# Optimization experiments

Hardware: AMD Instinct MI355X
Metric: run time of the kernel (lower is better)

The kernel has to match this reference:

```python
import jax, jax.numpy as jnp
import numpy as np

B, C, L, D = 8, 16, 512, 256  # batch, channels (attended axis), seq len, d_model


def setup_inputs() -> dict:
    key = jax.random.key(0)
    ks = jax.random.split(key, 9)
    d = D
    x = jax.random.normal(ks[0], (B, C, L, D), dtype=jnp.float32)
    # qkv projection: Linear(d, 3d), xavier_normal weight, zero-ish bias
    Wqkv = jax.random.normal(ks[1], (3 * d, d), dtype=jnp.float32) * (2.0 / (4 * d)) ** 0.5
    bqkv = jnp.zeros((3 * d,), dtype=jnp.float32)
    # additive-attention scorer V: Linear(d, 1)
    Vw = jax.random.normal(ks[2], (1, d), dtype=jnp.float32) * (1.0 / d) ** 0.5
    Vb = jnp.zeros((1,), dtype=jnp.float32)
    bh = jnp.zeros((d,), dtype=jnp.float32)  # nn.Parameter(torch.zeros(d_model))
    ba = jnp.zeros((1,), dtype=jnp.float32)  # nn.Parameter(torch.zeros(1))
    # output projection Linear(d, d)
    Wout = jax.random.normal(ks[3], (d, d), dtype=jnp.float32) * (1.0 / d) ** 0.5
    bout = jnp.zeros((d,), dtype=jnp.float32)
    return {"x": x, "Wqkv": Wqkv, "bqkv": bqkv, "Vw": Vw, "Vb": Vb,
            "bh": bh, "ba": ba, "Wout": Wout, "bout": bout}


def reference(x, Wqkv, bqkv, Vw, Vb, bh, ba, Wout, bout):
    b, c, l, d = x.shape
    # (b, c, l, d) -> (b*l, c, d): attention over the channel axis c per position
    xf = jnp.transpose(x, (0, 2, 1, 3)).reshape(b * l, c, d)
    qkv = xf @ Wqkv.T + bqkv                       # (B, c, 3d)
    q, k, v = jnp.split(qkv, 3, axis=-1)           # each (B, c, d)
    # additive (Bahdanau) score: V(tanh(q_i + k_j + bh)) + ba
    h = jnp.tanh(q[:, :, None, :] + k[:, None, :, :] + bh)  # (B, c, c, d)
    score = jnp.einsum('bqkd,d->bqk', h, Vw[0]) + Vb[0] + ba[0]  # (B, c, c)
    A = jax.nn.softmax(score, axis=-1)             # stable softmax (matches exp(s-max)/sum)
    # torch einsum 'b c c, b c d -> b c d': repeated index -> DIAGONAL of A scales v
    z = jnp.einsum('bcc,bcd->bcd', A, v)           # (B, c, d)
    z = z.reshape(b, l, c, d).transpose(0, 2, 1, 3)  # (b, c, l, d)
    return z @ Wout.T + bout
```

## Files before the change

kernel.cpp:

```cpp
#include <hip/hip_runtime.h>


typedef __attribute__((ext_vector_type(8))) short bf16x8;
typedef __attribute__((ext_vector_type(4))) float f32x4;
typedef __attribute__((ext_vector_type(8))) _Float16 h16x8;
typedef __attribute__((ext_vector_type(4))) _Float16 h16x4;
typedef const __attribute__((address_space(1))) void* gp1_t;
typedef __attribute__((address_space(3))) void* lp3_t;

__device__ __forceinline__ unsigned short f2bf(float f) {
  union { float f; unsigned int u; } v; v.f = f;
  return (unsigned short)((v.u + 0x7FFFu + ((v.u >> 16) & 1u)) >> 16);
}

__device__ __forceinline__ unsigned int cvt_pk_bf16(float a, float b) {
  unsigned int r;
  asm("v_cvt_pk_bf16_f32 %0, %1, %2" : "=v"(r) : "v"(a), "v"(b));
  return r;
}

__global__ __launch_bounds__(256) void ca_prep_kernel(
    const float* __restrict__ Wqkv, const float* __restrict__ Wout,
    const float* __restrict__ bqkv, const float* __restrict__ bh,
    unsigned short* __restrict__ Wqb_t, unsigned short* __restrict__ Wcb_t,
    float* __restrict__ bcomb, float* __restrict__ bsc) {
  const int blk = blockIdx.x;
  if (blk < 64) {
    const int t = blk * 256 + threadIdx.x;
    const int k8 = t >> 9, n = t & 511;
    const float* src = Wqkv + (size_t)n * 256 + k8 * 8;
    const float4 v0 = *(const float4*)src;
    const float4 v1 = *(const float4*)(src + 4);
    bf16x8 o;
    o[0] = (short)f2bf(v0.x); o[1] = (short)f2bf(v0.y);
    o[2] = (short)f2bf(v0.z); o[3] = (short)f2bf(v0.w);
    o[4] = (short)f2bf(v1.x); o[5] = (short)f2bf(v1.y);
    o[6] = (short)f2bf(v1.z); o[7] = (short)f2bf(v1.w);
    *(bf16x8*)(Wqb_t + (size_t)t * 8) = o;
    return;
  }
  const int dp = blk - 64;
  const int e = threadIdx.x;
  if (dp < 2) {
    const int n = dp * 256 + e;
    const float b = bqkv[n] + (n < 256 ? bh[n] : 0.f);
    bsc[n] = b * 2.8853900817779268f;
  }
  const float* wrow = Wout + (size_t)dp * 256;
  float acc = 0.f;
  for (int f = 0; f < 256; ++f)
    acc = fmaf(wrow[f], Wqkv[(size_t)(512 + f) * 256 + e], acc);
  Wcb_t[((size_t)(e >> 3) * 256 + dp) * 8 + (e & 7)] = f2bf(acc);
  if (e == 0) {
    float b = 0.f;
    for (int f = 0; f < 256; ++f) b = fmaf(wrow[f], bqkv[512 + f], b);
    bcomb[dp] = b;
  }
}

__global__ __launch_bounds__(512, 6) void ca_fused(
    const float* __restrict__ x,
    const unsigned short* __restrict__ Wqb_t,
    const unsigned short* __restrict__ Wcb_t,
    const float* __restrict__ bsc,
    const float* __restrict__ Vw,
    const float* __restrict__ bcomb, const float* __restrict__ bout,
    float* __restrict__ out) {
  __shared__ __align__(16) unsigned short xs[32 * 264];
  __shared__ __align__(16) unsigned short BsEs[16640];
  __shared__ __align__(16) float vw_s[256];
  __shared__ float af_s[32];
  unsigned short* const Bs = BsEs;
  _Float16* const Es = (_Float16*)BsEs;

  const int tid = threadIdx.x;
  const int lane = tid & 63, wave = tid >> 6;
  const int quad = lane >> 4, l15 = lane & 15;
  const int rt0 = blockIdx.x * 32;

  if (tid < 256) vw_s[tid] = -2.f * Vw[tid];

#pragma unroll
  for (int i = 0; i < 4; ++i) {
    const int sb = wave * 256 + i * 64;
    const unsigned short* g = Wqb_t + (size_t)(sb + lane) * 8;
    __builtin_amdgcn_global_load_lds((gp1_t)g, (lp3_t)(Bs + sb * 8), 16, 0, 0);
  }

  {
    const int rl = tid >> 4, c0 = (tid & 15) * 16;
    const int r = rt0 + rl;
    const int b = r >> 13, l = (r >> 4) & 511, c = r & 15;
    const float* src = x + ((size_t)(b * 16 + c) * 512 + l) * 256 + c0;
    unsigned short* dst = xs + rl * 264 + c0;
#pragma unroll
    for (int j = 0; j < 2; ++j) {
      const float4 v0 = *(const float4*)(src + j * 8);
      const float4 v1 = *(const float4*)(src + j * 8 + 4);
      uint4 o;
      o.x = cvt_pk_bf16(v0.x, v0.y);
      o.y = cvt_pk_bf16(v0.z, v0.w);
      o.z = cvt_pk_bf16(v1.x, v1.y);
      o.w = cvt_pk_bf16(v1.z, v1.w);
      *(uint4*)(dst + j * 8) = o;
    }
  }
  __syncthreads();

  f32x4 acc[2][4] = {};
  for (int k0c = 0; k0c < 8; ++k0c) {
    bf16x8 af[2], bfr[4];
#pragma unroll
    for (int mi = 0; mi < 2; ++mi)
      af[mi] = *(const bf16x8*)&xs[(mi * 16 + l15) * 264 + k0c * 32 + quad * 8];
#pragma unroll
    for (int ni = 0; ni < 4; ++ni)
      bfr[ni] = *(const bf16x8*)&Bs[(quad * 512 + wave * 64 + ni * 16 + l15) * 8];
    __syncthreads();
    if (k0c < 7) {
#pragma unroll
      for (int i = 0; i < 4; ++i) {
        const int sb = wave * 256 + i * 64;
        const unsigned short* g =
            Wqb_t + ((size_t)(k0c + 1) * 2048 + sb + lane) * 8;
        __builtin_amdgcn_global_load_lds((gp1_t)g, (lp3_t)(Bs + sb * 8), 16, 0, 0);
      }
    }
#pragma unroll
    for (int mi = 0; mi < 2; ++mi)
#pragma unroll
      for (int ni = 0; ni < 4; ++ni)
        acc[mi][ni] = __builtin_amdgcn_mfma_f32_16x16x32_bf16(
            bfr[ni], af[mi], acc[mi][ni], 0, 0, 0);
    __syncthreads();
  }

  const float SC = 2.8853900817779268f;
#pragma unroll
  for (int mi = 0; mi < 2; ++mi) {
    const int rl = mi * 16 + l15;
#pragma unroll
    for (int ni = 0; ni < 4; ++ni) {
      const int n = wave * 64 + ni * 16 + quad * 4;
      const float4 bs = *(const float4*)(bsc + n);
      h16x4 st;
      st[0] = (_Float16)__builtin_amdgcn_exp2f(
          fminf(15.f, fmaxf(-15.f, fmaf(acc[mi][ni][0], SC, bs.x))));
      st[1] = (_Float16)__builtin_amdgcn_exp2f(
          fminf(15.f, fmaxf(-15.f, fmaf(acc[mi][ni][1], SC, bs.y))));
      st[2] = (_Float16)__builtin_amdgcn_exp2f(
          fminf(15.f, fmaxf(-15.f, fmaf(acc[mi][ni][2], SC, bs.z))));
      st[3] = (_Float16)__builtin_amdgcn_exp2f(
          fminf(15.f, fmaxf(-15.f, fmaf(acc[mi][ni][3], SC, bs.w))));
      *(h16x4*)&Es[rl * 520 + n] = st;
    }
  }
  __syncthreads();

  f32x4 acc2[2][2] = {};
  {
    const int p = tid >> 8, qc = (tid >> 4) & 15, kc = tid & 15;
    const _Float16* eqp = Es + (p * 16 + qc) * 520;
    const _Float16* ekp = Es + (p * 16 + kc) * 520 + 256;
    const unsigned short* wb2 = Wcb_t + (size_t)(quad * 256 + wave * 32 + l15) * 8;
    bf16x8 bcur0 = *(const bf16x8*)(wb2);
    bf16x8 bcur1 = *(const bf16x8*)(wb2 + 128);
    f32x4 a4 = {};
#pragma unroll
    for (int c = 0; c < 8; ++c) {
      bf16x8 bnxt0, bnxt1;
      if (c < 7) {
        bnxt0 = *(const bf16x8*)(wb2 + (size_t)(c + 1) * 8192);
        bnxt1 = *(const bf16x8*)(wb2 + (size_t)(c + 1) * 8192 + 128);
      }
      bf16x8 af0 = *(const bf16x8*)&xs[l15 * 264 + c * 32 + quad * 8];
      bf16x8 af1 = *(const bf16x8*)&xs[(16 + l15) * 264 + c * 32 + quad * 8];
#pragma unroll
      for (int j = 0; j < 4; ++j) {
        const int d = c * 32 + j * 8;
        const h16x8 eq = *(const h16x8*)(eqp + d);
        const h16x8 ek = *(const h16x8*)(ekp + d);
        const f32x4 wv0 = *(const f32x4*)(vw_s + d);
        const f32x4 wv1 = *(const f32x4*)(vw_s + d + 4);
        f32x4 sg0, sg1;
        sg0.x = __builtin_amdgcn_rcpf(1.f + (float)eq[0] * (float)ek[0]);
        sg0.y = __builtin_amdgcn_rcpf(1.f + (float)eq[1] * (float)ek[1]);
        sg0.z = __builtin_amdgcn_rcpf(1.f + (float)eq[2] * (float)ek[2]);
        sg0.w = __builtin_amdgcn_rcpf(1.f + (float)eq[3] * (float)ek[3]);
        sg1.x = __builtin_amdgcn_rcpf(1.f + (float)eq[4] * (float)ek[4]);
        sg1.y = __builtin_amdgcn_rcpf(1.f + (float)eq[5] * (float)ek[5]);
        sg1.z = __builtin_amdgcn_rcpf(1.f + (float)eq[6] * (float)ek[6]);
        sg1.w = __builtin_amdgcn_rcpf(1.f + (float)eq[7] * (float)ek[7]);
        a4 += wv0 * sg0 + wv1 * sg1;
      }
      acc2[0][0] = __builtin_amdgcn_mfma_f32_16x16x32_bf16(bcur0, af0, acc2[0][0], 0, 0, 0);
      acc2[0][1] = __builtin_amdgcn_mfma_f32_16x16x32_bf16(bcur1, af0, acc2[0][1], 0, 0, 0);
      acc2[1][0] = __builtin_amdgcn_mfma_f32_16x16x32_bf16(bcur0, af1, acc2[1][0], 0, 0, 0);
      acc2[1][1] = __builtin_amdgcn_mfma_f32_16x16x32_bf16(bcur1, af1, acc2[1][1], 0, 0, 0);
      bcur0 = bnxt0; bcur1 = bnxt1;
    }
    float s = (a4[0] + a4[1]) + (a4[2] + a4[3]);
    float m = s;
    for (int off = 8; off; off >>= 1) m = fmaxf(m, __shfl_xor(m, off, 16));
    const float e = __builtin_amdgcn_exp2f((s - m) * 1.4426950408889634f);
    float sum = e;
    for (int off = 8; off; off >>= 1) sum += __shfl_xor(sum, off, 16);
    if (kc == qc) af_s[p * 16 + qc] = e / sum;
  }
  __syncthreads();

#pragma unroll
  for (int mi = 0; mi < 2; ++mi) {
    const int rl = mi * 16 + l15;
    const int r = rt0 + rl;
    const int c = r & 15, p = r >> 4;
    const int l = p & 511, b = p >> 9;
    const float av = af_s[rl];
    float* orow = out + ((size_t)(b * 16 + c) * 512 + l) * 256;
#pragma unroll
    for (int ni = 0; ni < 2; ++ni) {
      const int n = wave * 32 + ni * 16 + quad * 4;
      const float4 bc = *(const float4*)(bcomb + n);
      const float4 bo = *(const float4*)(bout + n);
      float4 o;
      o.x = fmaf(av, acc2[mi][ni][0] + bc.x, bo.x);
      o.y = fmaf(av, acc2[mi][ni][1] + bc.y, bo.y);
      o.z = fmaf(av, acc2[mi][ni][2] + bc.z, bo.z);
      o.w = fmaf(av, acc2[mi][ni][3] + bc.w, bo.w);
      *(float4*)(orow + n) = o;
    }
  }
}

extern "C" void kernel_launch(void* const* d_in, const int* in_sizes, int n_in,
                              void* d_out, int out_size, void* d_ws, size_t ws_size,
                              hipStream_t stream) {
  (void)in_sizes; (void)n_in; (void)out_size; (void)ws_size;
  const float* x    = (const float*)d_in[0];
  const float* Wqkv = (const float*)d_in[1];
  const float* bqkv = (const float*)d_in[2];
  const float* Vw   = (const float*)d_in[3];
  const float* bh   = (const float*)d_in[5];
  const float* Wout = (const float*)d_in[7];
  const float* bout = (const float*)d_in[8];
  float* out = (float*)d_out;

  float* bcomb = (float*)d_ws;
  float* bsc = bcomb + 256;
  unsigned short* Wqb_t = (unsigned short*)(bsc + 512);
  unsigned short* Wcb_t = Wqb_t + (size_t)512 * 256;

  ca_prep_kernel<<<dim3(320), dim3(256), 0, stream>>>(
      Wqkv, Wout, bqkv, bh, Wqb_t, Wcb_t, bcomb, bsc);
  ca_fused<<<dim3(2048), dim3(512), 0, stream>>>(
      x, Wqb_t, Wcb_t, bsc, Vw, bcomb, bout, out);
}
```

Before: 190.6 us.

## Double row tile to 64 rows per block with 1024 threads and 16 waves

Each block now handles 64 rows (4 positions) with 1024 threads, so each weight chunk staged in LDS is reused across twice as many rows. Waves cover narrower column slices (32 in the QKV GEMM, 16 in the output GEMM) but more M tiles. This cuts global weight traffic per row and halves the block count. In exchange LDS per block roughly doubles and the larger block may lower occupancy and add barrier cost.

```diff
diff --git a/kernel.cpp b/kernel.cpp
--- a/kernel.cpp
+++ b/kernel.cpp
@@ -58,7 +58,7 @@
   }
 }
 
-__global__ __launch_bounds__(512, 6) void ca_fused(
+__global__ __launch_bounds__(1024, 4) void ca_fused(
     const float* __restrict__ x,
     const unsigned short* __restrict__ Wqb_t,
     const unsigned short* __restrict__ Wcb_t,
@@ -66,25 +66,25 @@
     const float* __restrict__ Vw,
     const float* __restrict__ bcomb, const float* __restrict__ bout,
     float* __restrict__ out) {
-  __shared__ __align__(16) unsigned short xs[32 * 264];
-  __shared__ __align__(16) unsigned short BsEs[16640];
+  __shared__ __align__(16) unsigned short xs[64 * 264];
+  __shared__ __align__(16) unsigned short BsEs[33280];
   __shared__ __align__(16) float vw_s[256];
-  __shared__ float af_s[32];
+  __shared__ float af_s[64];
   unsigned short* const Bs = BsEs;
   _Float16* const Es = (_Float16*)BsEs;
 
   const int tid = threadIdx.x;
   const int lane = tid & 63, wave = tid >> 6;
   const int quad = lane >> 4, l15 = lane & 15;
-  const int rt0 = blockIdx.x * 32;
+  const int rt0 = blockIdx.x * 64;
 
   if (tid < 256) vw_s[tid] = -2.f * Vw[tid];
 
 #pragma unroll
-  for (int i = 0; i < 4; ++i) {
-    const int sb = wave * 256 + i * 64;
-    const unsigned short* g = Wqb_t + (size_t)(sb + lane) * 8;
-    __builtin_amdgcn_global_load_lds((gp1_t)g, (lp3_t)(Bs + sb * 8), 16, 0, 0);
+  for (int i = 0; i < 2; ++i) {
+    const int s = wave * 128 + i * 64 + lane;
+    const unsigned short* g = Wqb_t + (size_t)s * 8;
+    __builtin_amdgcn_global_load_lds((gp1_t)g, (lp3_t)(Bs + s * 8), 16, 0, 0);
   }
 
   {
@@ -107,29 +107,29 @@
   }
   __syncthreads();
 
-  f32x4 acc[2][4] = {};
+  f32x4 acc[4][2] = {};
   for (int k0c = 0; k0c < 8; ++k0c) {
-    bf16x8 af[2], bfr[4];
-#pragma unroll
-    for (int mi = 0; mi < 2; ++mi)
+    bf16x8 af[4], bfr[2];
+#pragma unroll
+    for (int mi = 0; mi < 4; ++mi)
       af[mi] = *(const bf16x8*)&xs[(mi * 16 + l15) * 264 + k0c * 32 + quad * 8];
 #pragma unroll
-    for (int ni = 0; ni < 4; ++ni)
-      bfr[ni] = *(const bf16x8*)&Bs[(quad * 512 + wave * 64 + ni * 16 + l15) * 8];
+    for (int ni = 0; ni < 2; ++ni)
+      bfr[ni] = *(const bf16x8*)&Bs[(quad * 512 + wave * 32 + ni * 16 + l15) * 8];
     __syncthreads();
     if (k0c < 7) {
 #pragma unroll
-      for (int i = 0; i < 4; ++i) {
-        const int sb = wave * 256 + i * 64;
+      for (int i = 0; i < 2; ++i) {
+        const int s = wave * 128 + i * 64 + lane;
         const unsigned short* g =
-            Wqb_t + ((size_t)(k0c + 1) * 2048 + sb + lane) * 8;
-        __builtin_amdgcn_global_load_lds((gp1_t)g, (lp3_t)(Bs + sb * 8), 16, 0, 0);
+            Wqb_t + ((size_t)(k0c + 1) * 2048 + s) * 8;
+        __builtin_amdgcn_global_load_lds((gp1_t)g, (lp3_t)(Bs + s * 8), 16, 0, 0);
       }
     }
 #pragma unroll
-    for (int mi = 0; mi < 2; ++mi)
-#pragma unroll
-      for (int ni = 0; ni < 4; ++ni)
+    for (int mi = 0; mi < 4; ++mi)
+#pragma unroll
+      for (int ni = 0; ni < 2; ++ni)
         acc[mi][ni] = __builtin_amdgcn_mfma_f32_16x16x32_bf16(
             bfr[ni], af[mi], acc[mi][ni], 0, 0, 0);
     __syncthreads();
@@ -137,11 +137,11 @@
 
   const float SC = 2.8853900817779268f;
 #pragma unroll
-  for (int mi = 0; mi < 2; ++mi) {
+  for (int mi = 0; mi < 4; ++mi) {
     const int rl = mi * 16 + l15;
 #pragma unroll
-    for (int ni = 0; ni < 4; ++ni) {
-      const int n = wave * 64 + ni * 16 + quad * 4;
+    for (int ni = 0; ni < 2; ++ni) {
+      const int n = wave * 32 + ni * 16 + quad * 4;
       const float4 bs = *(const float4*)(bsc + n);
       h16x4 st;
       st[0] = (_Float16)__builtin_amdgcn_exp2f(
@@ -157,24 +157,24 @@
   }
   __syncthreads();
 
-  f32x4 acc2[2][2] = {};
+  f32x4 acc2[4] = {};
   {
     const int p = tid >> 8, qc = (tid >> 4) & 15, kc = tid & 15;
     const _Float16* eqp = Es + (p * 16 + qc) * 520;
     const _Float16* ekp = Es + (p * 16 + kc) * 520 + 256;
-    const unsigned short* wb2 = Wcb_t + (size_t)(quad * 256 + wave * 32 + l15) * 8;
-    bf16x8 bcur0 = *(const bf16x8*)(wb2);
-    bf16x8 bcur1 = *(const bf16x8*)(wb2 + 128);
+    const unsigned short* wb2 = Wcb_t + (size_t)(quad * 256 + wave * 16 + l15) * 8;
+    bf16x8 bcur = *(const bf16x8*)(wb2);
     f32x4 a4 = {};
 #pragma unroll
     for (int c = 0; c < 8; ++c) {
-      bf16x8 bnxt0, bnxt1;
+      bf16x8 bnxt;
       if (c < 7) {
-        bnxt0 = *(const bf16x8*)(wb2 + (size_t)(c + 1) * 8192);
-        bnxt1 = *(const bf16x8*)(wb2 + (size_t)(c + 1) * 8192 + 128);
+        bnxt = *(const bf16x8*)(wb2 + (size_t)(c + 1) * 8192);
       }
-      bf16x8 af0 = *(const bf16x8*)&xs[l15 * 264 + c * 32 + quad * 8];
-      bf16x8 af1 = *(const bf16x8*)&xs[(16 + l15) * 264 + c * 32 + quad * 8];
+      bf16x8 af[4];
+#pragma unroll
+      for (int mi = 0; mi < 4; ++mi)
+        af[mi] = *(const bf16x8*)&xs[(mi * 16 + l15) * 264 + c * 32 + quad * 8];
 #pragma unroll
       for (int j = 0; j < 4; ++j) {
         const int d = c * 32 + j * 8;
@@ -193,11 +193,11 @@
         sg1.w = __builtin_amdgcn_rcpf(1.f + (float)eq[7] * (float)ek[7]);
         a4 += wv0 * sg0 + wv1 * sg1;
       }
-      acc2[0][0] = __builtin_amdgcn_mfma_f32_16x16x32_bf16(bcur0, af0, acc2[0][0], 0, 0, 0);
-      acc2[0][1] = __builtin_amdgcn_mfma_f32_16x16x32_bf16(bcur1, af0, acc2[0][1], 0, 0, 0);
-      acc2[1][0] = __builtin_amdgcn_mfma_f32_16x16x32_bf16(bcur0, af1, acc2[1][0], 0, 0, 0);
-      acc2[1][1] = __builtin_amdgcn_mfma_f32_16x16x32_bf16(bcur1, af1, acc2[1][1], 0, 0, 0);
-      bcur0 = bnxt0; bcur1 = bnxt1;
+      acc2[0] = __builtin_amdgcn_mfma_f32_16x16x32_bf16(bcur, af[0], acc2[0], 0, 0, 0);
+      acc2[1] = __builtin_amdgcn_mfma_f32_16x16x32_bf16(bcur, af[1], acc2[1], 0, 0, 0);
+      acc2[2] = __builtin_amdgcn_mfma_f32_16x16x32_bf16(bcur, af[2], acc2[2], 0, 0, 0);
+      acc2[3] = __builtin_amdgcn_mfma_f32_16x16x32_bf16(bcur, af[3], acc2[3], 0, 0, 0);
+      bcur = bnxt;
     }
     float s = (a4[0] + a4[1]) + (a4[2] + a4[3]);
     float m = s;
@@ -210,25 +210,22 @@
   __syncthreads();
 
 #pragma unroll
-  for (int mi = 0; mi < 2; ++mi) {
+  for (int mi = 0; mi < 4; ++mi) {
     const int rl = mi * 16 + l15;
     const int r = rt0 + rl;
     const int c = r & 15, p = r >> 4;
     const int l = p & 511, b = p >> 9;
     const float av = af_s[rl];
     float* orow = out + ((size_t)(b * 16 + c) * 512 + l) * 256;
-#pragma unroll
-    for (int ni = 0; ni < 2; ++ni) {
-      const int n = wave * 32 + ni * 16 + quad * 4;
-      const float4 bc = *(const float4*)(bcomb + n);
-      const float4 bo = *(const float4*)(bout + n);
-      float4 o;
-      o.x = fmaf(av, acc2[mi][ni][0] + bc.x, bo.x);
-      o.y = fmaf(av, acc2[mi][ni][1] + bc.y, bo.y);
-      o.z = fmaf(av, acc2[mi][ni][2] + bc.z, bo.z);
-      o.w = fmaf(av, acc2[mi][ni][3] + bc.w, bo.w);
-      *(float4*)(orow + n) = o;
-    }
+    const int n = wave * 16 + quad * 4;
+    const float4 bc = *(const float4*)(bcomb + n);
+    const float4 bo = *(const float4*)(bout + n);
+    float4 o;
+    o.x = fmaf(av, acc2[mi][0] + bc.x, bo.x);
+    o.y = fmaf(av, acc2[mi][1] + bc.y, bo.y);
+    o.z = fmaf(av, acc2[mi][2] + bc.z, bo.z);
+    o.w = fmaf(av, acc2[mi][3] + bc.w, bo.w);
+    *(float4*)(orow + n) = o;
   }
 }
 
@@ -252,6 +249,6 @@
 
   ca_prep_kernel<<<dim3(320), dim3(256), 0, stream>>>(
       Wqkv, Wout, bqkv, bh, Wqb_t, Wcb_t, bcomb, bsc);
-  ca_fused<<<dim3(2048), dim3(512), 0, stream>>>(
+  ca_fused<<<dim3(1024), dim3(1024), 0, stream>>>(
       x, Wqb_t, Wcb_t, bsc, Vw, bcomb, bout, out);
 }
```

Result: slower. 213.1 us (+11.8%).

## Process two row tiles per block, overlapping second tile's QK GEMM with first tile's scoring

Applied to the files above, without the earlier changes.

Each block now handles 64 rows as two 32-row halves. The first half's QK projection runs as before, while the second half's QK projection MFMAs are interleaved into the first half's score and output-projection loop. Those MFMAs read B fragments directly from global memory, not LDS. The aim is to hide the GEMM latency behind the VALU-heavy tanh/score computation and to halve the grid, at the cost of more registers (launch bounds lowered to 4 waves per SIMD), more LDS, and direct global weight loads.

```diff
diff --git a/kernel.cpp b/kernel.cpp
--- a/kernel.cpp
+++ b/kernel.cpp
@@ -58,7 +58,7 @@
   }
 }
 
-__global__ __launch_bounds__(512, 6) void ca_fused(
+__global__ __launch_bounds__(512, 4) void ca_fused(
     const float* __restrict__ x,
     const unsigned short* __restrict__ Wqb_t,
     const unsigned short* __restrict__ Wcb_t,
@@ -66,17 +66,18 @@
     const float* __restrict__ Vw,
     const float* __restrict__ bcomb, const float* __restrict__ bout,
     float* __restrict__ out) {
-  __shared__ __align__(16) unsigned short xs[32 * 264];
+  __shared__ __align__(16) unsigned short xs0[32 * 264];
+  __shared__ __align__(16) unsigned short xs1[32 * 264];
   __shared__ __align__(16) unsigned short BsEs[16640];
   __shared__ __align__(16) float vw_s[256];
-  __shared__ float af_s[32];
+  __shared__ float af_s[64];
   unsigned short* const Bs = BsEs;
   _Float16* const Es = (_Float16*)BsEs;
 
   const int tid = threadIdx.x;
   const int lane = tid & 63, wave = tid >> 6;
   const int quad = lane >> 4, l15 = lane & 15;
-  const int rt0 = blockIdx.x * 32;
+  const int rt0 = blockIdx.x * 64;
 
   if (tid < 256) vw_s[tid] = -2.f * Vw[tid];
 
@@ -89,20 +90,23 @@
 
   {
     const int rl = tid >> 4, c0 = (tid & 15) * 16;
-    const int r = rt0 + rl;
-    const int b = r >> 13, l = (r >> 4) & 511, c = r & 15;
-    const float* src = x + ((size_t)(b * 16 + c) * 512 + l) * 256 + c0;
-    unsigned short* dst = xs + rl * 264 + c0;
-#pragma unroll
-    for (int j = 0; j < 2; ++j) {
-      const float4 v0 = *(const float4*)(src + j * 8);
-      const float4 v1 = *(const float4*)(src + j * 8 + 4);
-      uint4 o;
-      o.x = cvt_pk_bf16(v0.x, v0.y);
-      o.y = cvt_pk_bf16(v0.z, v0.w);
-      o.z = cvt_pk_bf16(v1.x, v1.y);
-      o.w = cvt_pk_bf16(v1.z, v1.w);
-      *(uint4*)(dst + j * 8) = o;
+#pragma unroll
+    for (int h = 0; h < 2; ++h) {
+      const int r = rt0 + h * 32 + rl;
+      const int b = r >> 13, l = (r >> 4) & 511, cch = r & 15;
+      const float* src = x + ((size_t)(b * 16 + cch) * 512 + l) * 256 + c0;
+      unsigned short* dst = (h ? xs1 : xs0) + rl * 264 + c0;
+#pragma unroll
+      for (int j = 0; j < 2; ++j) {
+        const float4 v0 = *(const float4*)(src + j * 8);
+        const float4 v1 = *(const float4*)(src + j * 8 + 4);
+        uint4 o;
+        o.x = cvt_pk_bf16(v0.x, v0.y);
+        o.y = cvt_pk_bf16(v0.z, v0.w);
+        o.z = cvt_pk_bf16(v1.x, v1.y);
+        o.w = cvt_pk_bf16(v1.z, v1.w);
+        *(uint4*)(dst + j * 8) = o;
+      }
     }
   }
   __syncthreads();
@@ -112,7 +116,7 @@
     bf16x8 af[2], bfr[4];
 #pragma unroll
     for (int mi = 0; mi < 2; ++mi)
-      af[mi] = *(const bf16x8*)&xs[(mi * 16 + l15) * 264 + k0c * 32 + quad * 8];
+      af[mi] = *(const bf16x8*)&xs0[(mi * 16 + l15) * 264 + k0c * 32 + quad * 8];
 #pragma unroll
     for (int ni = 0; ni < 4; ++ni)
       bfr[ni] = *(const bf16x8*)&Bs[(quad * 512 + wave * 64 + ni * 16 + l15) * 8];
@@ -158,23 +162,26 @@
   __syncthreads();
 
   f32x4 acc2[2][2] = {};
+  f32x4 acc1p[2][4] = {};
   {
     const int p = tid >> 8, qc = (tid >> 4) & 15, kc = tid & 15;
     const _Float16* eqp = Es + (p * 16 + qc) * 520;
     const _Float16* ekp = Es + (p * 16 + kc) * 520 + 256;
     const unsigned short* wb2 = Wcb_t + (size_t)(quad * 256 + wave * 32 + l15) * 8;
-    bf16x8 bcur0 = *(const bf16x8*)(wb2);
-    bf16x8 bcur1 = *(const bf16x8*)(wb2 + 128);
+    const unsigned short* wq2 = Wqb_t + (size_t)(quad * 512 + wave * 64 + l15) * 8;
     f32x4 a4 = {};
 #pragma unroll
     for (int c = 0; c < 8; ++c) {
-      bf16x8 bnxt0, bnxt1;
-      if (c < 7) {
-        bnxt0 = *(const bf16x8*)(wb2 + (size_t)(c + 1) * 8192);
-        bnxt1 = *(const bf16x8*)(wb2 + (size_t)(c + 1) * 8192 + 128);
-      }
-      bf16x8 af0 = *(const bf16x8*)&xs[l15 * 264 + c * 32 + quad * 8];
-      bf16x8 af1 = *(const bf16x8*)&xs[(16 + l15) * 264 + c * 32 + quad * 8];
+      const bf16x8 b20 = *(const bf16x8*)(wb2 + (size_t)c * 8192);
+      const bf16x8 b21 = *(const bf16x8*)(wb2 + (size_t)c * 8192 + 128);
+      const bf16x8 b10 = *(const bf16x8*)(wq2 + (size_t)c * 16384);
+      const bf16x8 b11 = *(const bf16x8*)(wq2 + (size_t)c * 16384 + 128);
+      const bf16x8 b12 = *(const bf16x8*)(wq2 + (size_t)c * 16384 + 256);
+      const bf16x8 b13 = *(const bf16x8*)(wq2 + (size_t)c * 16384 + 384);
+      const bf16x8 a0 = *(const bf16x8*)&xs0[l15 * 264 + c * 32 + quad * 8];
+      const bf16x8 a1 = *(const bf16x8*)&xs0[(16 + l15) * 264 + c * 32 + quad * 8];
+      const bf16x8 q0 = *(const bf16x8*)&xs1[l15 * 264 + c * 32 + quad * 8];
+      const bf16x8 q1 = *(const bf16x8*)&xs1[(16 + l15) * 264 + c * 32 + quad * 8];
 #pragma unroll
       for (int j = 0; j < 4; ++j) {
         const int d = c * 32 + j * 8;
@@ -193,11 +200,18 @@
         sg1.w = __builtin_amdgcn_rcpf(1.f + (float)eq[7] * (float)ek[7]);
         a4 += wv0 * sg0 + wv1 * sg1;
       }
-      acc2[0][0] = __builtin_amdgcn_mfma_f32_16x16x32_bf16(bcur0, af0, acc2[0][0], 0, 0, 0);
-      acc2[0][1] = __builtin_amdgcn_mfma_f32_16x16x32_bf16(bcur1, af0, acc2[0][1], 0, 0, 0);
-      acc2[1][0] = __builtin_amdgcn_mfma_f32_16x16x32_bf16(bcur0, af1, acc2[1][0], 0, 0, 0);
-      acc2[1][1] = __builtin_amdgcn_mfma_f32_16x16x32_bf16(bcur1, af1, acc2[1][1], 0, 0, 0);
-      bcur0 = bnxt0; bcur1 = bnxt1;
+      acc2[0][0] = __builtin_amdgcn_mfma_f32_16x16x32_bf16(b20, a0, acc2[0][0], 0, 0, 0);
+      acc2[0][1] = __builtin_amdgcn_mfma_f32_16x16x32_bf16(b21, a0, acc2[0][1], 0, 0, 0);
+      acc2[1][0] = __builtin_amdgcn_mfma_f32_16x16x32_bf16(b20, a1, acc2[1][0], 0, 0, 0);
+      acc2[1][1] = __builtin_amdgcn_mfma_f32_16x16x32_bf16(b21, a1, acc2[1][1], 0, 0, 0);
+      acc1p[0][0] = __builtin_amdgcn_mfma_f32_16x16x32_bf16(b10, q0, acc1p[0][0], 0, 0, 0);
+      acc1p[0][1] = __builtin_amdgcn_mfma_f32_16x16x32_bf16(b11, q0, acc1p[0][1], 0, 0, 0);
+      acc1p[0][2] = __builtin_amdgcn_mfma_f32_16x16x32_bf16(b12, q0, acc1p[0][2], 0, 0, 0);
+      acc1p[0][3] = __builtin_amdgcn_mfma_f32_16x16x32_bf16(b13, q0, acc1p[0][3], 0, 0, 0);
+      acc1p[1][0] = __builtin_amdgcn_mfma_f32_16x16x32_bf16(b10, q1, acc1p[1][0], 0, 0, 0);
+      acc1p[1][1] = __builtin_amdgcn_mfma_f32_16x16x32_bf16(b11, q1, acc1p[1][1], 0, 0, 0);
+      acc1p[1][2] = __builtin_amdgcn_mfma_f32_16x16x32_bf16(b12, q1, acc1p[1][2], 0, 0, 0);
+      acc1p[1][3] = __builtin_amdgcn_mfma_f32_16x16x32_bf16(b13, q1, acc1p[1][3], 0, 0, 0);
     }
     float s = (a4[0] + a4[1]) + (a4[2] + a4[3]);
     float m = s;
@@ -213,10 +227,10 @@
   for (int mi = 0; mi < 2; ++mi) {
     const int rl = mi * 16 + l15;
     const int r = rt0 + rl;
-    const int c = r & 15, p = r >> 4;
-    const int l = p & 511, b = p >> 9;
+    const int cch = r & 15, pp = r >> 4;
+    const int l = pp & 511, b = pp >> 9;
     const float av = af_s[rl];
-    float* orow = out + ((size_t)(b * 16 + c) * 512 + l) * 256;
+    float* orow = out + ((size_t)(b * 16 + cch) * 512 + l) * 256;
 #pragma unroll
     for (int ni = 0; ni < 2; ++ni) {
       const int n = wave * 32 + ni * 16 + quad * 4;
@@ -227,6 +241,101 @@
       o.y = fmaf(av, acc2[mi][ni][1] + bc.y, bo.y);
       o.z = fmaf(av, acc2[mi][ni][2] + bc.z, bo.z);
       o.w = fmaf(av, acc2[mi][ni][3] + bc.w, bo.w);
+      *(float4*)(orow + n) = o;
+    }
+  }
+
+#pragma unroll
+  for (int mi = 0; mi < 2; ++mi) {
+    const int rl = mi * 16 + l15;
+#pragma unroll
+    for (int ni = 0; ni < 4; ++ni) {
+      const int n = wave * 64 + ni * 16 + quad * 4;
+      const float4 bs = *(const float4*)(bsc + n);
+      h16x4 st;
+      st[0] = (_Float16)__builtin_amdgcn_exp2f(
+          fminf(15.f, fmaxf(-15.f, fmaf(acc1p[mi][ni][0], SC, bs.x))));
+      st[1] = (_Float16)__builtin_amdgcn_exp2f(
+          fminf(15.f, fmaxf(-15.f, fmaf(acc1p[mi][ni][1], SC, bs.y))));
+      st[2] = (_Float16)__builtin_amdgcn_exp2f(
+          fminf(15.f, fmaxf(-15.f, fmaf(acc1p[mi][ni][2], SC, bs.z))));
+      st[3] = (_Float16)__builtin_amdgcn_exp2f(
+          fminf(15.f, fmaxf(-15.f, fmaf(acc1p[mi][ni][3], SC, bs.w))));
+      *(h16x4*)&Es[rl * 520 + n] = st;
+    }
+  }
+  __syncthreads();
+
+  f32x4 acc2b[2][2] = {};
+  {
+    const int p = tid >> 8, qc = (tid >> 4) & 15, kc = tid & 15;
+    const _Float16* eqp = Es + (p * 16 + qc) * 520;
+    const _Float16* ekp = Es + (p * 16 + kc) * 520 + 256;
+    const unsigned short* wb2 = Wcb_t + (size_t)(quad * 256 + wave * 32 + l15) * 8;
+    bf16x8 bcur0 = *(const bf16x8*)(wb2);
+    bf16x8 bcur1 = *(const bf16x8*)(wb2 + 128);
+    f32x4 a4 = {};
+#pragma unroll
+    for (int c = 0; c < 8; ++c) {
+      bf16x8 bnxt0, bnxt1;
+      if (c < 7) {
+        bnxt0 = *(const bf16x8*)(wb2 + (size_t)(c + 1) * 8192);
+        bnxt1 = *(const bf16x8*)(wb2 + (size_t)(c + 1) * 8192 + 128);
+      }
+      bf16x8 af0 = *(const bf16x8*)&xs1[l15 * 264 + c * 32 + quad * 8];
+      bf16x8 af1 = *(const bf16x8*)&xs1[(16 + l15) * 264 + c * 32 + quad * 8];
+#pragma unroll
+      for (int j = 0; j < 4; ++j) {
+        const int d = c * 32 + j * 8;
+        const h16x8 eq = *(const h16x8*)(eqp + d);
+        const h16x8 ek = *(const h16x8*)(ekp + d);
+        const f32x4 wv0 = *(const f32x4*)(vw_s + d);
+        const f32x4 wv1 = *(const f32x4*)(vw_s + d + 4);
+        f32x4 sg0, sg1;
+        sg0.x = __builtin_amdgcn_rcpf(1.f + (float)eq[0] * (float)ek[0]);
+        sg0.y = __builtin_amdgcn_rcpf(1.f + (float)eq[1] * (float)ek[1]);
+        sg0.z = __builtin_amdgcn_rcpf(1.f + (float)eq[2] * (float)ek[2]);
+        sg0.w = __builtin_amdgcn_rcpf(1.f + (float)eq[3] * (float)ek[3]);
+        sg1.x = __builtin_amdgcn_rcpf(1.f + (float)eq[4] * (float)ek[4]);
+        sg1.y = __builtin_amdgcn_rcpf(1.f + (float)eq[5] * (float)ek[5]);
+        sg1.z = __builtin_amdgcn_rcpf(1.f + (float)eq[6] * (float)ek[6]);
+        sg1.w = __builtin_amdgcn_rcpf(1.f + (float)eq[7] * (float)ek[7]);
+        a4 += wv0 * sg0 + wv1 * sg1;
+      }
+      acc2b[0][0] = __builtin_amdgcn_mfma_f32_16x16x32_bf16(bcur0, af0, acc2b[0][0], 0, 0, 0);
+      acc2b[0][1] = __builtin_amdgcn_mfma_f32_16x16x32_bf16(bcur1, af0, acc2b[0][1], 0, 0, 0);
+      acc2b[1][0] = __builtin_amdgcn_mfma_f32_16x16x32_bf16(bcur0, af1, acc2b[1][0], 0, 0, 0);
+      acc2b[1][1] = __builtin_amdgcn_mfma_f32_16x16x32_bf16(bcur1, af1, acc2b[1][1], 0, 0, 0);
+      bcur0 = bnxt0; bcur1 = bnxt1;
+    }
+    float s = (a4[0] + a4[1]) + (a4[2] + a4[3]);
+    float m = s;
+    for (int off = 8; off; off >>= 1) m = fmaxf(m, __shfl_xor(m, off, 16));
+    const float e = __builtin_amdgcn_exp2f((s - m) * 1.4426950408889634f);
+    float sum = e;
+    for (int off = 8; off; off >>= 1) sum += __shfl_xor(sum, off, 16);
+    if (kc == qc) af_s[32 + p * 16 + qc] = e / sum;
+  }
+  __syncthreads();
+
+#pragma unroll
+  for (int mi = 0; mi < 2; ++mi) {
+    const int rl = mi * 16 + l15;
+    const int r = rt0 + 32 + rl;
+    const int cch = r & 15, pp = r >> 4;
+    const int l = pp & 511, b = pp >> 9;
+    const float av = af_s[32 + rl];
+    float* orow = out + ((size_t)(b * 16 + cch) * 512 + l) * 256;
+#pragma unroll
+    for (int ni = 0; ni < 2; ++ni) {
+      const int n = wave * 32 + ni * 16 + quad * 4;
+      const float4 bc = *(const float4*)(bcomb + n);
+      const float4 bo = *(const float4*)(bout + n);
+      float4 o;
+      o.x = fmaf(av, acc2b[mi][ni][0] + bc.x, bo.x);
+      o.y = fmaf(av, acc2b[mi][ni][1] + bc.y, bo.y);
+      o.z = fmaf(av, acc2b[mi][ni][2] + bc.z, bo.z);
+      o.w = fmaf(av, acc2b[mi][ni][3] + bc.w, bo.w);
       *(float4*)(orow + n) = o;
     }
   }
@@ -252,6 +361,6 @@
 
   ca_prep_kernel<<<dim3(320), dim3(256), 0, stream>>>(
       Wqkv, Wout, bqkv, bh, Wqb_t, Wcb_t, bcomb, bsc);
-  ca_fused<<<dim3(2048), dim3(512), 0, stream>>>(
+  ca_fused<<<dim3(1024), dim3(512), 0, stream>>>(
       x, Wqb_t, Wcb_t, bsc, Vw, bcomb, bout, out);
 }
```

Measured after the change: 215.7 us. 13.2% more time.

## Load QKV weight fragments directly from global into registers with 3-stage prefetch

Applied to the files above, without the earlier changes.

Removes the LDS staging of the bf16 QKV weight tiles (global_load_lds plus two barriers per K-chunk). Each lane now loads its MFMA B-fragments straight from global memory into a 3-deep register ring buffer, prefetching two chunks ahead. This drops the per-iteration __syncthreads and the LDS round trip, but raises register pressure, so launch bounds occupancy is lowered from 6 to 4. Every block now reads the weights from global/L2 itself rather than through a cooperatively filled shared tile.

```diff
diff --git a/kernel.cpp b/kernel.cpp
--- a/kernel.cpp
+++ b/kernel.cpp
@@ -5,8 +5,6 @@
 typedef __attribute__((ext_vector_type(4))) float f32x4;
 typedef __attribute__((ext_vector_type(8))) _Float16 h16x8;
 typedef __attribute__((ext_vector_type(4))) _Float16 h16x4;
-typedef const __attribute__((address_space(1))) void* gp1_t;
-typedef __attribute__((address_space(3))) void* lp3_t;
 
 __device__ __forceinline__ unsigned short f2bf(float f) {
   union { float f; unsigned int u; } v; v.f = f;
@@ -58,7 +56,7 @@
   }
 }
 
-__global__ __launch_bounds__(512, 6) void ca_fused(
+__global__ __launch_bounds__(512, 4) void ca_fused(
     const float* __restrict__ x,
     const unsigned short* __restrict__ Wqb_t,
     const unsigned short* __restrict__ Wcb_t,
@@ -67,11 +65,10 @@
     const float* __restrict__ bcomb, const float* __restrict__ bout,
     float* __restrict__ out) {
   __shared__ __align__(16) unsigned short xs[32 * 264];
-  __shared__ __align__(16) unsigned short BsEs[16640];
+  __shared__ __align__(16) unsigned short EsB[16640];
   __shared__ __align__(16) float vw_s[256];
   __shared__ float af_s[32];
-  unsigned short* const Bs = BsEs;
-  _Float16* const Es = (_Float16*)BsEs;
+  _Float16* const Es = (_Float16*)EsB;
 
   const int tid = threadIdx.x;
   const int lane = tid & 63, wave = tid >> 6;
@@ -79,13 +76,6 @@
   const int rt0 = blockIdx.x * 32;
 
   if (tid < 256) vw_s[tid] = -2.f * Vw[tid];
-
-#pragma unroll
-  for (int i = 0; i < 4; ++i) {
-    const int sb = wave * 256 + i * 64;
-    const unsigned short* g = Wqb_t + (size_t)(sb + lane) * 8;
-    __builtin_amdgcn_global_load_lds((gp1_t)g, (lp3_t)(Bs + sb * 8), 16, 0, 0);
-  }
 
   {
     const int rl = tid >> 4, c0 = (tid & 15) * 16;
@@ -108,31 +98,33 @@
   __syncthreads();
 
   f32x4 acc[2][4] = {};
-  for (int k0c = 0; k0c < 8; ++k0c) {
-    bf16x8 af[2], bfr[4];
-#pragma unroll
-    for (int mi = 0; mi < 2; ++mi)
-      af[mi] = *(const bf16x8*)&xs[(mi * 16 + l15) * 264 + k0c * 32 + quad * 8];
-#pragma unroll
-    for (int ni = 0; ni < 4; ++ni)
-      bfr[ni] = *(const bf16x8*)&Bs[(quad * 512 + wave * 64 + ni * 16 + l15) * 8];
-    __syncthreads();
-    if (k0c < 7) {
-#pragma unroll
-      for (int i = 0; i < 4; ++i) {
-        const int sb = wave * 256 + i * 64;
-        const unsigned short* g =
-            Wqb_t + ((size_t)(k0c + 1) * 2048 + sb + lane) * 8;
-        __builtin_amdgcn_global_load_lds((gp1_t)g, (lp3_t)(Bs + sb * 8), 16, 0, 0);
+  {
+    const unsigned short* b1 = Wqb_t + quad * 4096 + (wave * 64 + l15) * 8;
+    bf16x8 bb[3][4];
+#pragma unroll
+    for (int s = 0; s < 2; ++s)
+#pragma unroll
+      for (int ni = 0; ni < 4; ++ni)
+        bb[s][ni] = *(const bf16x8*)(b1 + (size_t)s * 16384 + ni * 128);
+#pragma unroll
+    for (int c = 0; c < 8; ++c) {
+      if (c + 2 < 8) {
+#pragma unroll
+        for (int ni = 0; ni < 4; ++ni)
+          bb[(c + 2) % 3][ni] =
+              *(const bf16x8*)(b1 + (size_t)(c + 2) * 16384 + ni * 128);
       }
-    }
-#pragma unroll
-    for (int mi = 0; mi < 2; ++mi)
-#pragma unroll
-      for (int ni = 0; ni < 4; ++ni)
-        acc[mi][ni] = __builtin_amdgcn_mfma_f32_16x16x32_bf16(
-            bfr[ni], af[mi], acc[mi][ni], 0, 0, 0);
-    __syncthreads();
+      bf16x8 af[2];
+#pragma unroll
+      for (int mi = 0; mi < 2; ++mi)
+        af[mi] = *(const bf16x8*)&xs[(mi * 16 + l15) * 264 + c * 32 + quad * 8];
+#pragma unroll
+      for (int mi = 0; mi < 2; ++mi)
+#pragma unroll
+        for (int ni = 0; ni < 4; ++ni)
+          acc[mi][ni] = __builtin_amdgcn_mfma_f32_16x16x32_bf16(
+              bb[c % 3][ni], af[mi], acc[mi][ni], 0, 0, 0);
+    }
   }
 
   const float SC = 2.8853900817779268f;
```

New measurement: 187.7 us. About the same (-1.5%).
